# Kernel optimization log

Measured on AMD Instinct MI355X. Metric: run time of the kernel, lower is better.

The kernel has to match this reference:

```python
import jax, jax.numpy as jnp
import numpy as np

S, L, D = 512, 128, 256        # sents, sent_len, embedding_dim (= out_hidden, skip_rnn)
V, E_V, E_D = 50000, 10000, 64  # vocab, entity vocab, entity dim
B, P = 128, 16                  # batch examples, positions per example
H2, F = D // 2, 256             # attn hidden, feature_size


def setup_inputs() -> dict:
    key = jax.random.key(0)
    ks = jax.random.split(key, 16)
    emb = jax.random.normal(ks[0], (V, D), jnp.float32) * 0.02
    emb = emb.at[0].set(0.0)  # padding_idx=0
    ent_emb = jax.random.normal(ks[1], (E_V, E_D), jnp.float32) * 0.02
    ent_emb = ent_emb.at[0].set(0.0)
    x = jax.random.randint(ks[2], (S, L), 0, V)
    ents = jax.random.randint(ks[3], (B, 2), 0, E_V)
    spos = jax.random.randint(ks[4], (B, P, 2), 0, L)  # valid for both sent(<S) and tok(<L) axes
    tpos = jax.random.randint(ks[5], (B, P, 2), 0, L)
    attw_W = jax.random.normal(ks[6], (H2, D), jnp.float32) / np.sqrt(D)
    attw_b = jnp.zeros((H2,), jnp.float32)
    attw2_W = jax.random.normal(ks[7], (1, H2), jnp.float32) / np.sqrt(H2)
    FEAT = 2 * D + 2 * E_D
    cond_W = jax.random.normal(ks[8], (F, FEAT), jnp.float32) / np.sqrt(FEAT)
    cond_b = jnp.zeros((F,), jnp.float32)
    lin_W = jax.random.normal(ks[9], (2, F), jnp.float32) / np.sqrt(F)
    lin_b = jnp.zeros((2,), jnp.float32)
    return {"x": x, "ents": ents, "spos": spos, "tpos": tpos,
            "emb": emb, "ent_emb": ent_emb,
            "attw_W": attw_W, "attw_b": attw_b, "attw2_W": attw2_W,
            "cond_W": cond_W, "cond_b": cond_b, "lin_W": lin_W, "lin_b": lin_b}


def _attn_pool(h, attw_W, attw_b, attw2_W):
    # h: [B, P, D]  ->  [B, D]
    energy = jnp.tanh(jnp.einsum('bpd,hd->bph', h, attw_W) + attw_b)
    logits = jnp.einsum('bph,oh->bpo', energy, attw2_W)[..., 0]   # [B, P]
    w = jax.nn.softmax(logits, axis=1)
    return jnp.einsum('bp,bpd->bd', w, h)


def reference(x, ents, spos, tpos, emb, ent_emb, attw_W, attw_b, attw2_W,
              cond_W, cond_b, lin_W, lin_b):
    sent_hiddens = emb[x]                                  # [S, L, D] (skip_rnn path)
    s_h = sent_hiddens[spos[..., 0], spos[..., 1]]         # [B, P, D] ragged gather (batched)
    t_h = sent_hiddens[tpos[..., 0], tpos[..., 1]]         # [B, P, D]
    s_pool = _attn_pool(s_h, attw_W, attw_b, attw2_W)      # [B, D]
    t_pool = _attn_pool(t_h, attw_W, attw_b, attw2_W)      # [B, D]
    e_embs = ent_emb[ents].reshape(ents.shape[0], -1)      # [B, 2*E_D]
    feats = jnp.concatenate([s_pool, t_pool, e_embs], axis=-1)  # [B, 2D+2E_D]
    condensed = feats @ cond_W.T + cond_b                  # [B, F]
    score = jnp.tanh(condensed) @ lin_W.T + lin_b          # [B, 2]
    return score
```

## Files before the change

kernel.cpp:

```cpp
#include <hip/hip_runtime.h>

#define S_ 512
#define L_ 128
#define D_ 256
#define V_ 50000
#define EV_ 10000
#define ED_ 64
#define B_ 128
#define P_ 16
#define H2_ 128
#define F_ 256
#define FEAT_ 640
#define SH_STRIDE 264

__global__ __launch_bounds__(256) void pool_kernel(
    const int* __restrict__ x, const int* __restrict__ spos, const int* __restrict__ tpos,
    const float* __restrict__ emb,
    const float* __restrict__ attw_W, const float* __restrict__ attw_b,
    const float* __restrict__ attw2_W,
    float* __restrict__ ws_pool)
{
    const int bid = blockIdx.x;
    const int b = bid >> 1, pool = bid & 1;
    const int t = threadIdx.x;

    __shared__ float sh[P_ * SH_STRIDE];
    __shared__ float part[P_ * 256];
    __shared__ float wsum[4][8];
    __shared__ float wts[P_];

    {
        const int* pos = pool ? tpos : spos;
        const int p = t >> 4, i = t & 15;
        const int si  = pos[(b * P_ + p) * 2 + 0];
        const int ti  = pos[(b * P_ + p) * 2 + 1];
        const int tok = x[si * L_ + ti];
        const float4* row = (const float4*)(emb + (size_t)tok * D_);
        float* dst = &sh[p * SH_STRIDE + i * 16];
        #pragma unroll
        for (int j = 0; j < 4; ++j) {
            float4 v = row[i * 4 + j];
            dst[j * 4 + 0] = v.x; dst[j * 4 + 1] = v.y;
            dst[j * 4 + 2] = v.z; dst[j * 4 + 3] = v.w;
        }
    }
    __syncthreads();

    {
        const int h = t >> 1, dh = t & 1;
        const int d0 = dh * 128;
        const float4* awrow = (const float4*)(attw_W + (size_t)h * D_ + d0);
        float acc[P_];
        #pragma unroll
        for (int p = 0; p < P_; ++p) acc[p] = 0.f;
        float4 nxt = awrow[0];
        for (int c = 0; c < 32; ++c) {
            float4 a = nxt;
            if (c < 31) nxt = awrow[c + 1];
            const int d = d0 + c * 4;
            #pragma unroll
            for (int p = 0; p < P_; ++p) {
                float4 s = *(const float4*)&sh[p * SH_STRIDE + d];
                acc[p] += a.x * s.x + a.y * s.y + a.z * s.z + a.w * s.w;
            }
        }
        #pragma unroll
        for (int p = 0; p < P_; ++p) part[p * 256 + t] = acc[p];
    }
    __syncthreads();

    {
        const int h = t & 127, pg = t >> 7;
        const float bias = attw_b[h];
        const float w2   = attw2_W[h];
        float v[8];
        #pragma unroll
        for (int k = 0; k < 8; ++k) {
            const int p = pg * 8 + k;
            float e = part[p * 256 + 2 * h] + part[p * 256 + 2 * h + 1] + bias;
            v[k] = tanhf(e) * w2;
        }
        #pragma unroll
        for (int k = 0; k < 8; ++k) {
            float s = v[k];
            for (int m = 32; m >= 1; m >>= 1) s += __shfl_xor(s, m, 64);
            v[k] = s;
        }
        const int wid = t >> 6;
        if ((t & 63) == 0) {
            #pragma unroll
            for (int k = 0; k < 8; ++k) wsum[wid][k] = v[k];
        }
    }
    __syncthreads();

    if (t < P_) {
        const int pg = t >> 3, k = t & 7;
        float l = wsum[pg * 2][k] + wsum[pg * 2 + 1][k];
        float m = l;
        for (int mm = 8; mm >= 1; mm >>= 1) m = fmaxf(m, __shfl_xor(m, mm, 16));
        float e = expf(l - m);
        float ssum = e;
        for (int mm = 8; mm >= 1; mm >>= 1) ssum += __shfl_xor(ssum, mm, 16);
        wts[t] = e / ssum;
    }
    __syncthreads();

    {
        float acc = 0.f;
        #pragma unroll
        for (int p = 0; p < P_; ++p) acc += wts[p] * sh[p * SH_STRIDE + t];
        ws_pool[(size_t)b * 512 + pool * 256 + t] = acc;
    }
}

__global__ __launch_bounds__(256) void head_kernel(
    const int* __restrict__ ents,
    const float* __restrict__ ent_emb,
    const float* __restrict__ cond_W, const float* __restrict__ cond_b,
    const float* __restrict__ lin_W, const float* __restrict__ lin_b,
    const float* __restrict__ ws_pool,
    float* __restrict__ out)
{
    const int b = blockIdx.x, t = threadIdx.x;
    __shared__ float feats[FEAT_];
    __shared__ float r0[4], r1[4];

    feats[t]       = ws_pool[(size_t)b * 512 + t];
    feats[256 + t] = ws_pool[(size_t)b * 512 + 256 + t];
    if (t < 128) {
        const int e = ents[b * 2 + (t >> 6)];
        feats[512 + t] = ent_emb[(size_t)e * ED_ + (t & 63)];
    }
    __syncthreads();

    const float4* wrow = (const float4*)(cond_W + (size_t)t * FEAT_);
    float acc = cond_b[t];
    float4 nxt = wrow[0];
    for (int c = 0; c < 160; ++c) {
        float4 a = nxt;
        if (c < 159) nxt = wrow[c + 1];
        const float* fp = &feats[c * 4];
        acc += a.x * fp[0] + a.y * fp[1] + a.z * fp[2] + a.w * fp[3];
    }
    const float tv = tanhf(acc);
    float v0 = tv * lin_W[t];
    float v1 = tv * lin_W[256 + t];
    for (int m = 32; m >= 1; m >>= 1) {
        v0 += __shfl_xor(v0, m, 64);
        v1 += __shfl_xor(v1, m, 64);
    }
    if ((t & 63) == 0) { r0[t >> 6] = v0; r1[t >> 6] = v1; }
    __syncthreads();
    if (t == 0) {
        out[b * 2 + 0] = r0[0] + r0[1] + r0[2] + r0[3] + lin_b[0];
        out[b * 2 + 1] = r1[0] + r1[1] + r1[2] + r1[3] + lin_b[1];
    }
}

extern "C" void kernel_launch(void* const* d_in, const int* in_sizes, int n_in,
                              void* d_out, int out_size, void* d_ws, size_t ws_size,
                              hipStream_t stream)
{
    const int* x     = (const int*)d_in[0];
    const int* ents  = (const int*)d_in[1];
    const int* spos  = (const int*)d_in[2];
    const int* tpos  = (const int*)d_in[3];
    const float* emb     = (const float*)d_in[4];
    const float* ent_emb = (const float*)d_in[5];
    const float* attw_W  = (const float*)d_in[6];
    const float* attw_b  = (const float*)d_in[7];
    const float* attw2_W = (const float*)d_in[8];
    const float* cond_W  = (const float*)d_in[9];
    const float* cond_b  = (const float*)d_in[10];
    const float* lin_W   = (const float*)d_in[11];
    const float* lin_b   = (const float*)d_in[12];
    float* ws_pool = (float*)d_ws;
    float* out = (float*)d_out;

    pool_kernel<<<2 * B_, 256, 0, stream>>>(x, spos, tpos, emb, attw_W, attw_b, attw2_W, ws_pool);
    head_kernel<<<B_, 256, 0, stream>>>(ents, ent_emb, cond_W, cond_b, lin_W, lin_b, ws_pool, out);
}
```

Baseline: 141.0 us.

## Fuse pooling and head kernels with last-block atomic handoff, retile attention matvec

Merges the pool and head kernels into one launch. Each example's two pooling blocks bump a per-example atomic counter, and whichever block finishes second runs the head computation. The attention energy matvec is retiled so each thread computes 4 hidden units over strided float4 chunks, reduced with shuffles, which drops the large partial-sum shared buffer. The change adds a memset launch and atomic/fence overhead, and gives the second block of each pair a longer tail.

```diff
diff --git a/kernel.cpp b/kernel.cpp
--- a/kernel.cpp
+++ b/kernel.cpp
@@ -3,31 +3,37 @@
 #define S_ 512
 #define L_ 128
 #define D_ 256
-#define V_ 50000
-#define EV_ 10000
-#define ED_ 64
 #define B_ 128
 #define P_ 16
 #define H2_ 128
 #define F_ 256
 #define FEAT_ 640
+#define ED_ 64
 #define SH_STRIDE 264
+#define LP_STRIDE 65
 
-__global__ __launch_bounds__(256) void pool_kernel(
-    const int* __restrict__ x, const int* __restrict__ spos, const int* __restrict__ tpos,
-    const float* __restrict__ emb,
+__global__ __launch_bounds__(256) void fused_kernel(
+    const int* __restrict__ x, const int* __restrict__ ents,
+    const int* __restrict__ spos, const int* __restrict__ tpos,
+    const float* __restrict__ emb, const float* __restrict__ ent_emb,
     const float* __restrict__ attw_W, const float* __restrict__ attw_b,
     const float* __restrict__ attw2_W,
-    float* __restrict__ ws_pool)
+    const float* __restrict__ cond_W, const float* __restrict__ cond_b,
+    const float* __restrict__ lin_W, const float* __restrict__ lin_b,
+    float* __restrict__ ws_pool, int* __restrict__ counters,
+    float* __restrict__ out)
 {
     const int bid = blockIdx.x;
     const int b = bid >> 1, pool = bid & 1;
     const int t = threadIdx.x;
 
     __shared__ float sh[P_ * SH_STRIDE];
-    __shared__ float part[P_ * 256];
-    __shared__ float wsum[4][8];
+    __shared__ float lp[P_ * LP_STRIDE];
+    __shared__ float logits[P_];
     __shared__ float wts[P_];
+    __shared__ int   sflag;
+    __shared__ float feats[FEAT_];
+    __shared__ float r0s[4], r1s[4];
 
     {
         const int* pos = pool ? tpos : spos;
@@ -36,72 +42,83 @@
         const int ti  = pos[(b * P_ + p) * 2 + 1];
         const int tok = x[si * L_ + ti];
         const float4* row = (const float4*)(emb + (size_t)tok * D_);
-        float* dst = &sh[p * SH_STRIDE + i * 16];
+        float4* dst = (float4*)&sh[p * SH_STRIDE + i * 16];
         #pragma unroll
-        for (int j = 0; j < 4; ++j) {
-            float4 v = row[i * 4 + j];
-            dst[j * 4 + 0] = v.x; dst[j * 4 + 1] = v.y;
-            dst[j * 4 + 2] = v.z; dst[j * 4 + 3] = v.w;
+        for (int j = 0; j < 4; ++j) dst[j] = row[i * 4 + j];
+    }
+    __syncthreads();
+
+    {
+        const int hp = t >> 3, dh = t & 7;
+        const int h0 = hp * 4;
+        const float4* W4 = (const float4*)attw_W;
+        float acc[4][P_];
+        #pragma unroll
+        for (int q = 0; q < 4; ++q)
+            #pragma unroll
+            for (int p = 0; p < P_; ++p) acc[q][p] = 0.f;
+
+        float4 an[4];
+        #pragma unroll
+        for (int q = 0; q < 4; ++q) an[q] = W4[(h0 + q) * 64 + dh];
+
+        for (int c = 0; c < 8; ++c) {
+            float4 a[4];
+            #pragma unroll
+            for (int q = 0; q < 4; ++q) a[q] = an[q];
+            if (c < 7) {
+                #pragma unroll
+                for (int q = 0; q < 4; ++q) an[q] = W4[(h0 + q) * 64 + 8 * (c + 1) + dh];
+            }
+            const int d = (8 * c + dh) * 4;
+            #pragma unroll
+            for (int p = 0; p < P_; ++p) {
+                float4 s = *(const float4*)&sh[p * SH_STRIDE + d];
+                #pragma unroll
+                for (int q = 0; q < 4; ++q)
+                    acc[q][p] += a[q].x * s.x + a[q].y * s.y + a[q].z * s.z + a[q].w * s.w;
+            }
+        }
+
+        #pragma unroll
+        for (int m = 1; m <= 4; m <<= 1) {
+            #pragma unroll
+            for (int q = 0; q < 4; ++q)
+                #pragma unroll
+                for (int p = 0; p < P_; ++p)
+                    acc[q][p] += __shfl_xor(acc[q][p], m, 64);
+        }
+
+        const float b0 = attw_b[h0],     b1 = attw_b[h0 + 1];
+        const float b2 = attw_b[h0 + 2], b3 = attw_b[h0 + 3];
+        const float w0 = attw2_W[h0],     w1 = attw2_W[h0 + 1];
+        const float w2 = attw2_W[h0 + 2], w3 = attw2_W[h0 + 3];
+        #pragma unroll
+        for (int k = 0; k < 2; ++k) {
+            const int p = dh * 2 + k;
+            float v = tanhf(acc[0][p] + b0) * w0 + tanhf(acc[1][p] + b1) * w1
+                    + tanhf(acc[2][p] + b2) * w2 + tanhf(acc[3][p] + b3) * w3;
+            lp[p * LP_STRIDE + hp] = v;
         }
     }
     __syncthreads();
 
     {
-        const int h = t >> 1, dh = t & 1;
-        const int d0 = dh * 128;
-        const float4* awrow = (const float4*)(attw_W + (size_t)h * D_ + d0);
-        float acc[P_];
+        const int p = t >> 4, g = t & 15;
+        float s = lp[p * LP_STRIDE + 2 * g] + lp[p * LP_STRIDE + 2 * g + 1];
         #pragma unroll
-        for (int p = 0; p < P_; ++p) acc[p] = 0.f;
-        float4 nxt = awrow[0];
-        for (int c = 0; c < 32; ++c) {
-            float4 a = nxt;
-            if (c < 31) nxt = awrow[c + 1];
-            const int d = d0 + c * 4;
-            #pragma unroll
-            for (int p = 0; p < P_; ++p) {
-                float4 s = *(const float4*)&sh[p * SH_STRIDE + d];
-                acc[p] += a.x * s.x + a.y * s.y + a.z * s.z + a.w * s.w;
-            }
-        }
-        #pragma unroll
-        for (int p = 0; p < P_; ++p) part[p * 256 + t] = acc[p];
-    }
-    __syncthreads();
-
-    {
-        const int h = t & 127, pg = t >> 7;
-        const float bias = attw_b[h];
-        const float w2   = attw2_W[h];
-        float v[8];
-        #pragma unroll
-        for (int k = 0; k < 8; ++k) {
-            const int p = pg * 8 + k;
-            float e = part[p * 256 + 2 * h] + part[p * 256 + 2 * h + 1] + bias;
-            v[k] = tanhf(e) * w2;
-        }
-        #pragma unroll
-        for (int k = 0; k < 8; ++k) {
-            float s = v[k];
-            for (int m = 32; m >= 1; m >>= 1) s += __shfl_xor(s, m, 64);
-            v[k] = s;
-        }
-        const int wid = t >> 6;
-        if ((t & 63) == 0) {
-            #pragma unroll
-            for (int k = 0; k < 8; ++k) wsum[wid][k] = v[k];
-        }
+        for (int m = 1; m <= 8; m <<= 1) s += __shfl_xor(s, m, 64);
+        if (g == 0) logits[p] = s;
     }
     __syncthreads();
 
     if (t < P_) {
-        const int pg = t >> 3, k = t & 7;
-        float l = wsum[pg * 2][k] + wsum[pg * 2 + 1][k];
+        float l = logits[t];
         float m = l;
-        for (int mm = 8; mm >= 1; mm >>= 1) m = fmaxf(m, __shfl_xor(m, mm, 16));
+        for (int mm = 8; mm >= 1; mm >>= 1) m = fmaxf(m, __shfl_xor(m, mm, 64));
         float e = expf(l - m);
         float ssum = e;
-        for (int mm = 8; mm >= 1; mm >>= 1) ssum += __shfl_xor(ssum, mm, 16);
+        for (int mm = 8; mm >= 1; mm >>= 1) ssum += __shfl_xor(ssum, mm, 64);
         wts[t] = e / ssum;
     }
     __syncthreads();
@@ -112,19 +129,15 @@
         for (int p = 0; p < P_; ++p) acc += wts[p] * sh[p * SH_STRIDE + t];
         ws_pool[(size_t)b * 512 + pool * 256 + t] = acc;
     }
-}
 
-__global__ __launch_bounds__(256) void head_kernel(
-    const int* __restrict__ ents,
-    const float* __restrict__ ent_emb,
-    const float* __restrict__ cond_W, const float* __restrict__ cond_b,
-    const float* __restrict__ lin_W, const float* __restrict__ lin_b,
-    const float* __restrict__ ws_pool,
-    float* __restrict__ out)
-{
-    const int b = blockIdx.x, t = threadIdx.x;
-    __shared__ float feats[FEAT_];
-    __shared__ float r0[4], r1[4];
+    __threadfence();
+    if (t == 0) {
+        int old = atomicAdd(&counters[b], 1);
+        sflag = (old == 1);
+    }
+    __syncthreads();
+    if (!sflag) return;
+    __threadfence();
 
     feats[t]       = ws_pool[(size_t)b * 512 + t];
     feats[256 + t] = ws_pool[(size_t)b * 512 + 256 + t];
@@ -150,11 +163,11 @@
         v0 += __shfl_xor(v0, m, 64);
         v1 += __shfl_xor(v1, m, 64);
     }
-    if ((t & 63) == 0) { r0[t >> 6] = v0; r1[t >> 6] = v1; }
+    if ((t & 63) == 0) { r0s[t >> 6] = v0; r1s[t >> 6] = v1; }
     __syncthreads();
     if (t == 0) {
-        out[b * 2 + 0] = r0[0] + r0[1] + r0[2] + r0[3] + lin_b[0];
-        out[b * 2 + 1] = r1[0] + r1[1] + r1[2] + r1[3] + lin_b[1];
+        out[b * 2 + 0] = r0s[0] + r0s[1] + r0s[2] + r0s[3] + lin_b[0];
+        out[b * 2 + 1] = r1s[0] + r1s[1] + r1s[2] + r1s[3] + lin_b[1];
     }
 }
 
@@ -176,8 +189,11 @@
     const float* lin_W   = (const float*)d_in[11];
     const float* lin_b   = (const float*)d_in[12];
     float* ws_pool = (float*)d_ws;
+    int* counters  = (int*)((char*)d_ws + 256 * 1024);
     float* out = (float*)d_out;
 
-    pool_kernel<<<2 * B_, 256, 0, stream>>>(x, spos, tpos, emb, attw_W, attw_b, attw2_W, ws_pool);
-    head_kernel<<<B_, 256, 0, stream>>>(ents, ent_emb, cond_W, cond_b, lin_W, lin_b, ws_pool, out);
+    hipMemsetAsync(counters, 0, B_ * sizeof(int), stream);
+    fused_kernel<<<2 * B_, 256, 0, stream>>>(
+        x, ents, spos, tpos, emb, ent_emb, attw_W, attw_b, attw2_W,
+        cond_W, cond_b, lin_W, lin_b, ws_pool, counters, out);
 }
```

Result: slower. 176.4 us (+25.2%).
